# Kernel tuning notes

Hardware: AMD Instinct MI355X
Metric: run time of the kernel (lower is better)

The kernel has to match this reference:

```python
import jax, jax.numpy as jnp
import numpy as np


def setup_inputs() -> dict:
    key = jax.random.key(0)
    k1, k2, *kw = jax.random.split(key, 12)
    N, E = 10000, 320000
    D_IN, D_HID, D_EMB, D_PRED = 2, 128, 256, 128

    def lin(k, fan_in, fan_out):
        bound = 1.0 / np.sqrt(fan_in)
        kw_, kb_ = jax.random.split(k)
        W = jax.random.uniform(kw_, (fan_in, fan_out), jnp.float32, -bound, bound)
        b = jax.random.uniform(kb_, (fan_out,), jnp.float32, -bound, bound)
        return W, b

    W1, b1 = lin(kw[0], D_IN, D_HID)
    W2, b2 = lin(kw[1], D_HID, D_EMB)
    Wp1, bp1 = lin(kw[2], D_EMB, D_PRED)
    Wp2, bp2 = lin(kw[3], D_PRED, 1)

    src = jax.random.randint(k1, (E,), 0, N, dtype=jnp.int32)
    dst = jax.random.randint(k2, (E,), 0, N, dtype=jnp.int32)
    return {
        "W1": W1, "b1": b1, "W2": W2, "b2": b2,
        "Wp1": Wp1, "bp1": bp1, "Wp2": Wp2, "bp2": bp2,
        "src": src, "dst": dst, "num_nodes": N,
    }


def reference(W1, b1, W2, b2, Wp1, bp1, Wp2, bp2, src, dst, num_nodes):
    N = num_nodes
    E = src.shape[0]
    ones = jnp.ones((E,), jnp.float32)
    # node features = [in_degree, out_degree]  -> [N, 2]
    in_deg = jax.ops.segment_sum(ones, dst, num_segments=N)
    out_deg = jax.ops.segment_sum(ones, src, num_segments=N)
    x = jnp.stack([in_deg, out_deg], axis=1)

    def gcn_agg(h):
        # sum of messages from source nodes into destination nodes (SpMM-like)
        return jax.ops.segment_sum(h[src], dst, num_segments=N)

    h = jax.nn.relu(gcn_agg(x) @ W1 + b1)        # [N, 128]
    h = gcn_agg(h) @ W2 + b2                     # [N, 256]
    h = jax.nn.relu(h)
    graph_embedding = jnp.sum(h, axis=0)         # [256] (dgl.sum_nodes, single graph)
    m = jax.nn.relu(graph_embedding @ Wp1 + bp1)
    metric = m @ Wp2 + bp2                       # [1]
    return (graph_embedding, metric)
```

## Files before the change

### kernel.cpp

```cpp
#include <hip/hip_runtime.h>

#define N_NODES 10000
#define CAPLOG 7
#define CAP 128
#define NPART 16
#define NBH 128
#define TBH 512
#define NSEG 8
#define SEGW 16

__global__ __launch_bounds__(TBH) void hist_kernel(const int* __restrict__ src,
                                                   const int* __restrict__ dst,
                                                   unsigned int* __restrict__ cnt,
                                                   float* __restrict__ ge_p, int E) {
  __shared__ unsigned int hist[N_NODES];
  const int tid = threadIdx.x, bid = blockIdx.x;
  if (bid == 0)
    for (int i = tid; i < NPART * 256; i += TBH) ge_p[i] = 0.f;
  for (int i = tid; i < N_NODES; i += TBH) hist[i] = 0;
  __syncthreads();
  const int chunk = (E + NBH - 1) / NBH;
  const int e0 = bid * chunk, e1 = min(E, e0 + chunk);
  for (int e = e0 + tid; e < e1; e += TBH) {
    atomicAdd(&hist[dst[e]], 1u);
    atomicAdd(&hist[src[e]], 0x10000u);
  }
  __syncthreads();
  unsigned int* outb = cnt + (size_t)bid * N_NODES;
  for (int i = tid; i < N_NODES; i += TBH) outb[i] = hist[i];
}

__global__ __launch_bounds__(256) void scan1_kernel(const unsigned int* __restrict__ cnt,
                                                    unsigned int* __restrict__ off,
                                                    unsigned int* __restrict__ psum) {
  const int n = blockIdx.x * 256 + threadIdx.x;
  const int seg = blockIdx.y;
  if (n >= N_NODES) return;
  unsigned run = 0;
  for (int i = 0; i < SEGW; ++i) {
    const size_t idx = (size_t)(seg * SEGW + i) * N_NODES + n;
    unsigned v = cnt[idx];
    off[idx] = run;
    run += v;
  }
  psum[(size_t)seg * N_NODES + n] = run;
}

__global__ __launch_bounds__(256) void scan2_kernel(const unsigned int* __restrict__ psum,
                                                    unsigned int* __restrict__ sbase,
                                                    unsigned int* __restrict__ pack) {
  const int n = blockIdx.x * 256 + threadIdx.x;
  if (n >= N_NODES) return;
  unsigned base = 0;
#pragma unroll
  for (int seg = 0; seg < NSEG; ++seg) {
    sbase[(size_t)seg * N_NODES + n] = base;
    base += psum[(size_t)seg * N_NODES + n];
  }
  pack[n] = base;
}

__global__ __launch_bounds__(TBH) void scatter_kernel(const int* __restrict__ src,
                                                      const int* __restrict__ dst,
                                                      const unsigned int* __restrict__ off,
                                                      const unsigned int* __restrict__ sbase,
                                                      unsigned short* __restrict__ slots,
                                                      int E) {
  __shared__ unsigned int cur[N_NODES];
  const int tid = threadIdx.x, bid = blockIdx.x;
  const unsigned int* ob = off + (size_t)bid * N_NODES;
  const unsigned int* sb = sbase + (size_t)(bid / SEGW) * N_NODES;
  for (int i = tid; i < N_NODES; i += TBH)
    cur[i] = (ob[i] & 0xFFFFu) + (sb[i] & 0xFFFFu);
  __syncthreads();
  const int chunk = (E + NBH - 1) / NBH;
  const int e0 = bid * chunk, e1 = min(E, e0 + chunk);
  for (int e = e0 + tid; e < e1; e += TBH) {
    int d = dst[e];
    unsigned idx = atomicAdd(&cur[d], 1u);
    if (idx < CAP) slots[(d << CAPLOG) + idx] = (unsigned short)src[e];
  }
}

__global__ __launch_bounds__(256) void agg1_kernel(const unsigned int* __restrict__ pack,
                                                   const unsigned short* __restrict__ slots,
                                                   float2* __restrict__ a) {
  const int tid = threadIdx.x;
  const int hw = tid >> 5, hl = tid & 31;
  const int node = blockIdx.x * 8 + hw;
  const int deg = min((int)(pack[node] & 0xFFFFu), CAP);
  const int base = node << CAPLOG;
  float a0 = 0.f, a1 = 0.f;
  for (int e = hl; e < deg; e += 32) {
    unsigned v = pack[slots[base + e]];
    a0 += (float)(v & 0xFFFFu);
    a1 += (float)(v >> 16);
  }
#pragma unroll
  for (int o = 16; o > 0; o >>= 1) {
    a0 += __shfl_xor(a0, o);
    a1 += __shfl_xor(a1, o);
  }
  if (hl == 0) a[node] = make_float2(a0, a1);
}

__global__ __launch_bounds__(256) void agg2gemm2_kernel(const unsigned int* __restrict__ pack,
                                                        const unsigned short* __restrict__ slots,
                                                        const float2* __restrict__ a,
                                                        const float* __restrict__ W1,
                                                        const float* __restrict__ b1,
                                                        const float* __restrict__ W2,
                                                        const float* __restrict__ b2,
                                                        float* __restrict__ ge_p) {
  __shared__ float s_tile[16][128];
  const int tid = threadIdx.x, bid = blockIdx.x;
  const int hw = tid >> 5, hl = tid & 31;

  float w10[4], w11[4], bb[4];
#pragma unroll
  for (int c = 0; c < 4; ++c) {
    w10[c] = W1[4 * hl + c];
    w11[c] = W1[128 + 4 * hl + c];
    bb[c] = b1[4 * hl + c];
  }
#pragma unroll
  for (int jn = 0; jn < 2; ++jn) {
    const int node = bid * 16 + hw * 2 + jn;
    const int deg = min((int)(pack[node] & 0xFFFFu), CAP);
    float acc0 = 0.f, acc1 = 0.f, acc2 = 0.f, acc3 = 0.f;
    int rem = deg, eb = node << CAPLOG;
    while (rem > 0) {
      int cnt = min(rem, 32);
      float va0 = 0.f, va1 = 0.f;
      if (hl < cnt) {
        float2 av = a[slots[eb + hl]];
        va0 = av.x;
        va1 = av.y;
      }
      for (int jj = 0; jj < cnt; ++jj) {
        float x0 = __shfl(va0, jj, 32);
        float x1 = __shfl(va1, jj, 32);
        acc0 += fmaxf(fmaf(x0, w10[0], fmaf(x1, w11[0], bb[0])), 0.f);
        acc1 += fmaxf(fmaf(x0, w10[1], fmaf(x1, w11[1], bb[1])), 0.f);
        acc2 += fmaxf(fmaf(x0, w10[2], fmaf(x1, w11[2], bb[2])), 0.f);
        acc3 += fmaxf(fmaf(x0, w10[3], fmaf(x1, w11[3], bb[3])), 0.f);
      }
      rem -= cnt;
      eb += cnt;
    }
    s_tile[hw * 2 + jn][4 * hl + 0] = acc0;
    s_tile[hw * 2 + jn][4 * hl + 1] = acc1;
    s_tile[hw * 2 + jn][4 * hl + 2] = acc2;
    s_tile[hw * 2 + jn][4 * hl + 3] = acc3;
  }
  __syncthreads();

  const int qt = tid >> 6;
  const int c4 = (tid & 63) * 4;
  float d[4][4];
#pragma unroll
  for (int r = 0; r < 4; ++r)
#pragma unroll
    for (int c = 0; c < 4; ++c) d[r][c] = 0.f;
#pragma unroll
  for (int kc = 0; kc < 8; ++kc) {
    float4 wv[16];
#pragma unroll
    for (int c = 0; c < 16; ++c)
      wv[c] = *(const float4*)&W2[(kc * 16 + c) * 256 + c4];
#pragma unroll
    for (int r = 0; r < 4; ++r) {
      const float4* row4 = (const float4*)&s_tile[4 * qt + r][kc * 16];
#pragma unroll
      for (int q = 0; q < 4; ++q) {
        float4 rv = row4[q];
#pragma unroll
        for (int c = 0; c < 4; ++c) {
          d[r][c] = fmaf(rv.x, wv[4 * q + 0].x * 0.f + (&wv[4 * q + 0].x)[c], d[r][c]);
        }
      }
    }
  }
#pragma unroll
  for (int r = 0; r < 4; ++r)
#pragma unroll
    for (int c = 0; c < 4; ++c) d[r][c] = 0.f;
#pragma unroll
  for (int kc = 0; kc < 8; ++kc) {
    float4 wv[16];
#pragma unroll
    for (int c = 0; c < 16; ++c)
      wv[c] = *(const float4*)&W2[(kc * 16 + c) * 256 + c4];
#pragma unroll
    for (int r = 0; r < 4; ++r) {
      const float4* row4 = (const float4*)&s_tile[4 * qt + r][kc * 16];
#pragma unroll
      for (int q = 0; q < 4; ++q) {
        float4 rv = row4[q];
        float4 w0 = wv[4 * q + 0], w1 = wv[4 * q + 1], w2v = wv[4 * q + 2], w3 = wv[4 * q + 3];
        d[r][0] = fmaf(rv.x, w0.x, d[r][0]); d[r][1] = fmaf(rv.x, w0.y, d[r][1]);
        d[r][2] = fmaf(rv.x, w0.z, d[r][2]); d[r][3] = fmaf(rv.x, w0.w, d[r][3]);
        d[r][0] = fmaf(rv.y, w1.x, d[r][0]); d[r][1] = fmaf(rv.y, w1.y, d[r][1]);
        d[r][2] = fmaf(rv.y, w1.z, d[r][2]); d[r][3] = fmaf(rv.y, w1.w, d[r][3]);
        d[r][0] = fmaf(rv.z, w2v.x, d[r][0]); d[r][1] = fmaf(rv.z, w2v.y, d[r][1]);
        d[r][2] = fmaf(rv.z, w2v.z, d[r][2]); d[r][3] = fmaf(rv.z, w2v.w, d[r][3]);
        d[r][0] = fmaf(rv.w, w3.x, d[r][0]); d[r][1] = fmaf(rv.w, w3.y, d[r][1]);
        d[r][2] = fmaf(rv.w, w3.z, d[r][2]); d[r][3] = fmaf(rv.w, w3.w, d[r][3]);
      }
    }
  }

  const int part = (bid & (NPART - 1)) << 8;
#pragma unroll
  for (int c = 0; c < 4; ++c) {
    const float bj = b2[c4 + c];
    float g = 0.f;
#pragma unroll
    for (int r = 0; r < 4; ++r) g += fmaxf(d[r][c] + bj, 0.f);
    atomicAdd(&ge_p[part + c4 + c], g);
  }
}

__global__ __launch_bounds__(256) void head_kernel(const float* __restrict__ ge_p,
                                                   const float* __restrict__ Wp1,
                                                   const float* __restrict__ bp1,
                                                   const float* __restrict__ Wp2,
                                                   const float* __restrict__ bp2,
                                                   float* __restrict__ out) {
  __shared__ float s_ge[256];
  __shared__ float s_m[256];
  int tid = threadIdx.x;
  float g = 0.f;
#pragma unroll
  for (int p = 0; p < NPART; ++p) g += ge_p[p * 256 + tid];
  s_ge[tid] = g;
  out[tid] = g;
  __syncthreads();
  int j = tid & 127, halfk = tid >> 7;
  float d = halfk ? 0.f : bp1[j];
  int k0 = halfk << 7;
#pragma unroll 8
  for (int k = k0; k < k0 + 128; ++k) d = fmaf(s_ge[k], Wp1[k * 128 + j], d);
  s_m[tid] = d;
  __syncthreads();
  if (tid < 128) s_m[tid] = fmaxf(s_m[tid] + s_m[tid + 128], 0.f) * Wp2[tid];
  __syncthreads();
  if (tid < 64) {
    float v = s_m[tid] + s_m[tid + 64];
#pragma unroll
    for (int off = 32; off > 0; off >>= 1) v += __shfl_xor(v, off);
    if (tid == 0) out[256] = v + bp2[0];
  }
}

extern "C" void kernel_launch(void* const* d_in, const int* in_sizes, int n_in,
                              void* d_out, int out_size, void* d_ws, size_t ws_size,
                              hipStream_t stream) {
  const float* W1 = (const float*)d_in[0];
  const float* b1 = (const float*)d_in[1];
  const float* W2 = (const float*)d_in[2];
  const float* b2 = (const float*)d_in[3];
  const float* Wp1 = (const float*)d_in[4];
  const float* bp1 = (const float*)d_in[5];
  const float* Wp2 = (const float*)d_in[6];
  const float* bp2 = (const float*)d_in[7];
  const int* src = (const int*)d_in[8];
  const int* dst = (const int*)d_in[9];
  const int E = in_sizes[8];
  const int N = N_NODES;

  char* p = (char*)d_ws;
  float* ge_p = (float*)p;               p += (size_t)NPART * 256 * 4;
  unsigned int* pack = (unsigned int*)p; p += (size_t)N * 4;
  unsigned short* slots = (unsigned short*)p; p += (size_t)N * CAP * 2;
  float2* a = (float2*)p;                p += (size_t)N * 8;
  unsigned int* cnt = (unsigned int*)p;  p += (size_t)NBH * N * 4;
  unsigned int* off = (unsigned int*)p;  p += (size_t)NBH * N * 4;
  unsigned int* psum = (unsigned int*)p; p += (size_t)NSEG * N * 4;
  unsigned int* sbase = (unsigned int*)p;
  float* out = (float*)d_out;

  hist_kernel<<<NBH, TBH, 0, stream>>>(src, dst, cnt, ge_p, E);
  scan1_kernel<<<dim3((N + 255) / 256, NSEG), 256, 0, stream>>>(cnt, off, psum);
  scan2_kernel<<<(N + 255) / 256, 256, 0, stream>>>(psum, sbase, pack);
  scatter_kernel<<<NBH, TBH, 0, stream>>>(src, dst, off, sbase, slots, E);
  agg1_kernel<<<N / 8, 256, 0, stream>>>(pack, slots, a);
  agg2gemm2_kernel<<<N / 16, 256, 0, stream>>>(pack, slots, a, W1, b1, W2, b2, ge_p);
  head_kernel<<<1, 256, 0, stream>>>(ge_p, Wp1, bp1, Wp2, bp2, out);
}
```

Measured before the change: 142.3 us.

## Drop redundant GEMM pass and retile agg2gemm2 to 8 nodes per block

Removes a dummy first GEMM pass whose results were discarded, so the W2 multiply runs once per block. Each block now handles 8 nodes, with one wavefront-half per node, and the GEMM is retiled so each thread computes 4 rows by 2 output columns. This doubles the grid size and raises parallelism, at the cost of doubling total W2 reads and atomic adds into the partial graph embedding.

```diff
diff --git a/kernel.cpp b/kernel.cpp
--- a/kernel.cpp
+++ b/kernel.cpp
@@ -112,7 +112,7 @@
                                                         const float* __restrict__ W2,
                                                         const float* __restrict__ b2,
                                                         float* __restrict__ ge_p) {
-  __shared__ float s_tile[16][128];
+  __shared__ float s_tile[8][128];
   const int tid = threadIdx.x, bid = blockIdx.x;
   const int hw = tid >> 5, hl = tid & 31;
 
@@ -123,102 +123,72 @@
     w11[c] = W1[128 + 4 * hl + c];
     bb[c] = b1[4 * hl + c];
   }
-#pragma unroll
-  for (int jn = 0; jn < 2; ++jn) {
-    const int node = bid * 16 + hw * 2 + jn;
-    const int deg = min((int)(pack[node] & 0xFFFFu), CAP);
-    float acc0 = 0.f, acc1 = 0.f, acc2 = 0.f, acc3 = 0.f;
-    int rem = deg, eb = node << CAPLOG;
-    while (rem > 0) {
-      int cnt = min(rem, 32);
-      float va0 = 0.f, va1 = 0.f;
-      if (hl < cnt) {
-        float2 av = a[slots[eb + hl]];
-        va0 = av.x;
-        va1 = av.y;
-      }
-      for (int jj = 0; jj < cnt; ++jj) {
-        float x0 = __shfl(va0, jj, 32);
-        float x1 = __shfl(va1, jj, 32);
-        acc0 += fmaxf(fmaf(x0, w10[0], fmaf(x1, w11[0], bb[0])), 0.f);
-        acc1 += fmaxf(fmaf(x0, w10[1], fmaf(x1, w11[1], bb[1])), 0.f);
-        acc2 += fmaxf(fmaf(x0, w10[2], fmaf(x1, w11[2], bb[2])), 0.f);
-        acc3 += fmaxf(fmaf(x0, w10[3], fmaf(x1, w11[3], bb[3])), 0.f);
-      }
-      rem -= cnt;
-      eb += cnt;
+  const int node = bid * 8 + hw;
+  const int deg = min((int)(pack[node] & 0xFFFFu), CAP);
+  float acc0 = 0.f, acc1 = 0.f, acc2 = 0.f, acc3 = 0.f;
+  int rem = deg, eb = node << CAPLOG;
+  while (rem > 0) {
+    int cnt = min(rem, 32);
+    float va0 = 0.f, va1 = 0.f;
+    if (hl < cnt) {
+      float2 av = a[slots[eb + hl]];
+      va0 = av.x;
+      va1 = av.y;
     }
-    s_tile[hw * 2 + jn][4 * hl + 0] = acc0;
-    s_tile[hw * 2 + jn][4 * hl + 1] = acc1;
-    s_tile[hw * 2 + jn][4 * hl + 2] = acc2;
-    s_tile[hw * 2 + jn][4 * hl + 3] = acc3;
-  }
-  __syncthreads();
-
-  const int qt = tid >> 6;
-  const int c4 = (tid & 63) * 4;
-  float d[4][4];
-#pragma unroll
-  for (int r = 0; r < 4; ++r)
-#pragma unroll
-    for (int c = 0; c < 4; ++c) d[r][c] = 0.f;
-#pragma unroll
-  for (int kc = 0; kc < 8; ++kc) {
-    float4 wv[16];
-#pragma unroll
-    for (int c = 0; c < 16; ++c)
-      wv[c] = *(const float4*)&W2[(kc * 16 + c) * 256 + c4];
+    for (int jj = 0; jj < cnt; ++jj) {
+      float x0 = __shfl(va0, jj, 32);
+      float x1 = __shfl(va1, jj, 32);
+      acc0 += fmaxf(fmaf(x0, w10[0], fmaf(x1, w11[0], bb[0])), 0.f);
+      acc1 += fmaxf(fmaf(x0, w10[1], fmaf(x1, w11[1], bb[1])), 0.f);
+      acc2 += fmaxf(fmaf(x0, w10[2], fmaf(x1, w11[2], bb[2])), 0.f);
+      acc3 += fmaxf(fmaf(x0, w10[3], fmaf(x1, w11[3], bb[3])), 0.f);
+    }
+    rem -= cnt;
+    eb += cnt;
+  }
+  s_tile[hw][4 * hl + 0] = acc0;
+  s_tile[hw][4 * hl + 1] = acc1;
+  s_tile[hw][4 * hl + 2] = acc2;
+  s_tile[hw][4 * hl + 3] = acc3;
+  __syncthreads();
+
+  const int rg = tid >> 7;
+  const int c2 = (tid & 127) * 2;
+  float d0[4], d1[4];
+#pragma unroll
+  for (int r = 0; r < 4; ++r) { d0[r] = 0.f; d1[r] = 0.f; }
+#pragma unroll
+  for (int kc = 0; kc < 4; ++kc) {
+    float2 wv[32];
+#pragma unroll
+    for (int cc = 0; cc < 32; ++cc)
+      wv[cc] = *(const float2*)&W2[(kc * 32 + cc) * 256 + c2];
 #pragma unroll
     for (int r = 0; r < 4; ++r) {
-      const float4* row4 = (const float4*)&s_tile[4 * qt + r][kc * 16];
-#pragma unroll
-      for (int q = 0; q < 4; ++q) {
+      const float4* row4 = (const float4*)&s_tile[4 * rg + r][kc * 32];
+#pragma unroll
+      for (int q = 0; q < 8; ++q) {
         float4 rv = row4[q];
-#pragma unroll
-        for (int c = 0; c < 4; ++c) {
-          d[r][c] = fmaf(rv.x, wv[4 * q + 0].x * 0.f + (&wv[4 * q + 0].x)[c], d[r][c]);
-        }
+        float2 wa = wv[4 * q + 0], wb = wv[4 * q + 1];
+        float2 wc = wv[4 * q + 2], wd = wv[4 * q + 3];
+        d0[r] = fmaf(rv.x, wa.x, d0[r]); d1[r] = fmaf(rv.x, wa.y, d1[r]);
+        d0[r] = fmaf(rv.y, wb.x, d0[r]); d1[r] = fmaf(rv.y, wb.y, d1[r]);
+        d0[r] = fmaf(rv.z, wc.x, d0[r]); d1[r] = fmaf(rv.z, wc.y, d1[r]);
+        d0[r] = fmaf(rv.w, wd.x, d0[r]); d1[r] = fmaf(rv.w, wd.y, d1[r]);
       }
     }
   }
-#pragma unroll
-  for (int r = 0; r < 4; ++r)
-#pragma unroll
-    for (int c = 0; c < 4; ++c) d[r][c] = 0.f;
-#pragma unroll
-  for (int kc = 0; kc < 8; ++kc) {
-    float4 wv[16];
-#pragma unroll
-    for (int c = 0; c < 16; ++c)
-      wv[c] = *(const float4*)&W2[(kc * 16 + c) * 256 + c4];
-#pragma unroll
-    for (int r = 0; r < 4; ++r) {
-      const float4* row4 = (const float4*)&s_tile[4 * qt + r][kc * 16];
-#pragma unroll
-      for (int q = 0; q < 4; ++q) {
-        float4 rv = row4[q];
-        float4 w0 = wv[4 * q + 0], w1 = wv[4 * q + 1], w2v = wv[4 * q + 2], w3 = wv[4 * q + 3];
-        d[r][0] = fmaf(rv.x, w0.x, d[r][0]); d[r][1] = fmaf(rv.x, w0.y, d[r][1]);
-        d[r][2] = fmaf(rv.x, w0.z, d[r][2]); d[r][3] = fmaf(rv.x, w0.w, d[r][3]);
-        d[r][0] = fmaf(rv.y, w1.x, d[r][0]); d[r][1] = fmaf(rv.y, w1.y, d[r][1]);
-        d[r][2] = fmaf(rv.y, w1.z, d[r][2]); d[r][3] = fmaf(rv.y, w1.w, d[r][3]);
-        d[r][0] = fmaf(rv.z, w2v.x, d[r][0]); d[r][1] = fmaf(rv.z, w2v.y, d[r][1]);
-        d[r][2] = fmaf(rv.z, w2v.z, d[r][2]); d[r][3] = fmaf(rv.z, w2v.w, d[r][3]);
-        d[r][0] = fmaf(rv.w, w3.x, d[r][0]); d[r][1] = fmaf(rv.w, w3.y, d[r][1]);
-        d[r][2] = fmaf(rv.w, w3.z, d[r][2]); d[r][3] = fmaf(rv.w, w3.w, d[r][3]);
-      }
-    }
-  }
-
+
+  const float bj0 = b2[c2], bj1 = b2[c2 + 1];
+  float g0 = 0.f, g1 = 0.f;
+#pragma unroll
+  for (int r = 0; r < 4; ++r) {
+    g0 += fmaxf(d0[r] + bj0, 0.f);
+    g1 += fmaxf(d1[r] + bj1, 0.f);
+  }
   const int part = (bid & (NPART - 1)) << 8;
-#pragma unroll
-  for (int c = 0; c < 4; ++c) {
-    const float bj = b2[c4 + c];
-    float g = 0.f;
-#pragma unroll
-    for (int r = 0; r < 4; ++r) g += fmaxf(d[r][c] + bj, 0.f);
-    atomicAdd(&ge_p[part + c4 + c], g);
-  }
+  atomicAdd(&ge_p[part + c2], g0);
+  atomicAdd(&ge_p[part + c2 + 1], g1);
 }
 
 __global__ __launch_bounds__(256) void head_kernel(const float* __restrict__ ge_p,
@@ -285,6 +255,6 @@
   scan2_kernel<<<(N + 255) / 256, 256, 0, stream>>>(psum, sbase, pack);
   scatter_kernel<<<NBH, TBH, 0, stream>>>(src, dst, off, sbase, slots, E);
   agg1_kernel<<<N / 8, 256, 0, stream>>>(pack, slots, a);
-  agg2gemm2_kernel<<<N / 16, 256, 0, stream>>>(pack, slots, a, W1, b1, W2, b2, ge_p);
+  agg2gemm2_kernel<<<N / 8, 256, 0, stream>>>(pack, slots, a, W1, b1, W2, b2, ge_p);
   head_kernel<<<1, 256, 0, stream>>>(ge_p, Wp1, bp1, Wp2, bp2, out);
 }
```

New measurement: 135.9 us. 4.5% less time.
